# Kernel optimization log

Measured on AMD Instinct MI355X. Metric: run time of the kernel, lower is better.

The kernel has to match this reference:

```python
import jax, jax.numpy as jnp
import numpy as np

EPS = 1e-5

def _bn(x, g, b):
    # training-mode BatchNorm1d: batch statistics (biased variance), eps=1e-5
    mean = jnp.mean(x, axis=0)
    var = jnp.mean(jnp.square(x - mean), axis=0)
    return (x - mean) * jax.lax.rsqrt(var + EPS) * g + b

def setup_inputs() -> dict:
    key = jax.random.key(0)
    ks = jax.random.split(key, 16)
    n_nodes, n_edges, d_h, d_e = 50000, 800000, 128, 64
    in_feats, h1, h2, out_feats = 2 * d_h + d_e, 256, 128, 1
    def lin(k, fi, fo):
        bound = 1.0 / np.sqrt(fi)
        kw, kb = jax.random.split(k)
        W = jax.random.uniform(kw, (fo, fi), jnp.float32, -bound, bound)
        b = jax.random.uniform(kb, (fo,), jnp.float32, -bound, bound)
        return W, b
    W1, b1 = lin(ks[0], in_feats, h1)
    W2, b2 = lin(ks[1], h1, h2)
    W3, b3 = lin(ks[2], h2, out_feats)
    return {
        "h": jax.random.normal(ks[3], (n_nodes, d_h), jnp.float32),
        "e": jax.random.normal(ks[4], (n_edges, d_e), jnp.float32),
        "src": jax.random.randint(ks[5], (n_edges,), 0, n_nodes, jnp.int32),
        "dst": jax.random.randint(ks[6], (n_edges,), 0, n_nodes, jnp.int32),
        "bn0_g": jnp.ones((in_feats,), jnp.float32), "bn0_b": jnp.zeros((in_feats,), jnp.float32),
        "W1": W1, "b1": b1,
        "bn1_g": jnp.ones((h1,), jnp.float32), "bn1_b": jnp.zeros((h1,), jnp.float32),
        "W2": W2, "b2": b2,
        "bn2_g": jnp.ones((h2,), jnp.float32), "bn2_b": jnp.zeros((h2,), jnp.float32),
        "W3": W3, "b3": b3,
    }

def reference(h, e, src, dst, bn0_g, bn0_b, W1, b1, bn1_g, bn1_b, W2, b2, bn2_g, bn2_b, W3, b3):
    # edge gather + concat: [n_edges, 2*d_h + d_e]
    x = jnp.concatenate([h[src], h[dst], e], axis=1)
    x = _bn(x, bn0_g, bn0_b)
    x = jnp.maximum(x @ W1.T + b1, 0.0)  # Linear + ReLU (dropout = identity, deterministic)
    x = _bn(x, bn1_g, bn1_b)
    x = jnp.maximum(x @ W2.T + b2, 0.0)
    x = _bn(x, bn2_g, bn2_b)
    return x @ W3.T + b3
```

## Files before the change

### kernel.cpp

```cpp
#include <hip/hip_runtime.h>


#define N_EDGES 800000
#define N_NODES 50000

typedef __attribute__((ext_vector_type(8))) short bf8_t;
typedef __attribute__((ext_vector_type(4))) float f4_t;
typedef __attribute__((ext_vector_type(2))) unsigned int u2_t;
typedef __attribute__((ext_vector_type(4))) unsigned int u4_t;

__device__ __forceinline__ unsigned short f2bf(float f) {
    unsigned int u = __builtin_bit_cast(unsigned int, f);
    u += 0x7FFFu + ((u >> 16) & 1u);
    return (unsigned short)(u >> 16);
}
__device__ __forceinline__ float bf2f(unsigned short s) {
    unsigned int u = ((unsigned int)s) << 16;
    return __builtin_bit_cast(float, u);
}
__device__ __forceinline__ bf8_t cvt8(f4_t x, f4_t y) {
    bf8_t r;
    r[0] = (short)f2bf(x[0]); r[1] = (short)f2bf(x[1]);
    r[2] = (short)f2bf(x[2]); r[3] = (short)f2bf(x[3]);
    r[4] = (short)f2bf(y[0]); r[5] = (short)f2bf(y[1]);
    r[6] = (short)f2bf(y[2]); r[7] = (short)f2bf(y[3]);
    return r;
}

__global__ __launch_bounds__(256) void k_hist(const int* __restrict__ src, const int* __restrict__ dst,
                                              int* __restrict__ cs, int* __restrict__ cd) {
    int i = blockIdx.x * 256 + threadIdx.x;
    if (i < N_EDGES) {
        atomicAdd(&cs[src[i]], 1);
        atomicAdd(&cd[dst[i]], 1);
    }
}

__global__ __launch_bounds__(256) void k_ecvt(const float* __restrict__ e,
        unsigned short* __restrict__ ebf, float* __restrict__ sum, float* __restrict__ sq) {
    const int tid = threadIdx.x;
    const int lane = tid & 63;
    const int cg = tid & 7, rr = tid >> 3;
    f4_t sa = {0.f,0.f,0.f,0.f}, sb = sa, qa = sa, qb = sa;
    for (int r = blockIdx.x * 32 + rr; r < N_EDGES; r += gridDim.x * 32) {
        f4_t va = __builtin_nontemporal_load((const f4_t*)(e + (size_t)r * 64 + cg * 8));
        f4_t vb = __builtin_nontemporal_load((const f4_t*)(e + (size_t)r * 64 + cg * 8 + 4));
        sa += va; qa += va * va; sb += vb; qb += vb * vb;
        bf8_t o = cvt8(va, vb);
        __builtin_nontemporal_store(o,
            (bf8_t*)(ebf + (size_t)(r >> 4) * 1024 + (cg >> 2) * 512 + (((r & 15) << 2) + (cg & 3)) * 8));
    }
#pragma unroll
    for (int d = 8; d <= 32; d <<= 1) {
#pragma unroll
        for (int j = 0; j < 4; ++j) {
            sa[j] += __shfl_xor(sa[j], d); qa[j] += __shfl_xor(qa[j], d);
            sb[j] += __shfl_xor(sb[j], d); qb[j] += __shfl_xor(qb[j], d);
        }
    }
    __shared__ float red[128];
    if (tid < 128) red[tid] = 0.f;
    __syncthreads();
    if (lane < 8) {
#pragma unroll
        for (int j = 0; j < 4; ++j) {
            atomicAdd(&red[lane * 8 + j], sa[j]);
            atomicAdd(&red[lane * 8 + 4 + j], sb[j]);
            atomicAdd(&red[64 + lane * 8 + j], qa[j]);
            atomicAdd(&red[64 + lane * 8 + 4 + j], qb[j]);
        }
    }
    __syncthreads();
    if (tid < 64) atomicAdd(&sum[256 + tid], red[tid]);
    else if (tid < 128) atomicAdd(&sq[256 + tid - 64], red[tid]);
}

__global__ __launch_bounds__(256) void k_hstats(const float* __restrict__ h,
                                                const int* __restrict__ cs, const int* __restrict__ cd,
                                                float* __restrict__ sum, float* __restrict__ sq) {
    const int tid = threadIdx.x;
    const int c = tid & 127, g = tid >> 7;
    float ss = 0.f, qs = 0.f, sd = 0.f, qd = 0.f;
    for (int n = blockIdx.x * 2 + g; n < N_NODES; n += gridDim.x * 2) {
        float v = h[(size_t)n * 128 + c];
        float a = (float)cs[n], b = (float)cd[n];
        ss += a * v; qs += a * v * v;
        sd += b * v; qd += b * v * v;
    }
    __shared__ float red[256];
    red[tid] = ss; __syncthreads();
    if (tid < 128) atomicAdd(&sum[tid], red[tid] + red[tid + 128]);
    __syncthreads();
    red[tid] = qs; __syncthreads();
    if (tid < 128) atomicAdd(&sq[tid], red[tid] + red[tid + 128]);
    __syncthreads();
    red[tid] = sd; __syncthreads();
    if (tid < 128) atomicAdd(&sum[128 + tid], red[tid] + red[tid + 128]);
    __syncthreads();
    red[tid] = qd; __syncthreads();
    if (tid < 128) atomicAdd(&sq[128 + tid], red[tid] + red[tid + 128]);
}

__global__ __launch_bounds__(320) void k_fold0(const float* __restrict__ sum, const float* __restrict__ sq,
        const float* __restrict__ g0, const float* __restrict__ b0,
        float* __restrict__ scale0, float* __restrict__ shift0) {
    int j = threadIdx.x;
    if (j < 320) {
        const float invE = 1.f / (float)N_EDGES;
        float mu = sum[j] * invE;
        float var = sq[j] * invE - mu * mu;
        float sc = g0[j] * rsqrtf(var + 1e-5f);
        scale0[j] = sc;
        shift0[j] = b0[j] - mu * sc;
    }
}

__global__ __launch_bounds__(320) void k_foldW1(const float* __restrict__ W1, const float* __restrict__ b1,
        const float* __restrict__ scale0, const float* __restrict__ shift0,
        unsigned short* __restrict__ W1s, unsigned short* __restrict__ W1d,
        unsigned short* __restrict__ W1e, float* __restrict__ b1p) {
    __shared__ float sc[320], sh[320];
    const int tid = threadIdx.x;
    if (tid < 320) { sc[tid] = scale0[tid]; sh[tid] = shift0[tid]; }
    __syncthreads();
    if (tid < 256) {
        float acc = b1[tid];
        const float* wr = W1 + (size_t)tid * 320;
        for (int j = 0; j < 320; ++j) {
            float wv = wr[j];
            acc += wv * sh[j];
            unsigned short wb = f2bf(wv * sc[j]);
            if (j < 128) W1s[tid * 128 + j] = wb;
            else if (j < 256) W1d[tid * 128 + (j - 128)] = wb;
            else W1e[tid * 64 + (j - 256)] = wb;
        }
        b1p[tid] = acc;
    }
}

__global__ __launch_bounds__(256) void k_P(const float* __restrict__ h,
        const unsigned short* __restrict__ W1s, const unsigned short* __restrict__ W1d,
        unsigned short* __restrict__ Ps, unsigned short* __restrict__ Pd) {
    __shared__ unsigned short tile[16 * 264];
    const int tid = threadIdx.x;
    const int w = tid >> 6, lane = tid & 63, quad = lane >> 4, l15 = lane & 15;
    const unsigned short* W = blockIdx.y ? W1d : W1s;
    unsigned short* P = blockIdx.y ? Pd : Ps;
    const size_t base = (size_t)blockIdx.x * 256;
    bf8_t bfr[4][4];
#pragma unroll
    for (int j = 0; j < 4; ++j) {
        const unsigned short* wp = W + (size_t)((w * 4 + j) * 16 + l15) * 128 + quad * 8;
#pragma unroll
        for (int ks = 0; ks < 4; ++ks) bfr[j][ks] = *(const bf8_t*)(wp + ks * 32);
    }
    const int erow = tid >> 4, ex = tid & 15;
    for (int mc = 0; mc < 16; ++mc) {
        const size_t row0 = base + mc * 16;
        size_t ar = row0 + l15; if (ar >= N_NODES) ar = N_NODES - 1;
        const float* hp = h + ar * 128 + quad * 8;
        bf8_t af[4];
#pragma unroll
        for (int ks = 0; ks < 4; ++ks)
            af[ks] = cvt8(*(const f4_t*)(hp + ks * 32), *(const f4_t*)(hp + ks * 32 + 4));
#pragma unroll
        for (int j = 0; j < 4; ++j) {
            f4_t t = {0.f, 0.f, 0.f, 0.f};
#pragma unroll
            for (int ks = 0; ks < 4; ++ks)
                t = __builtin_amdgcn_mfma_f32_16x16x32_bf16(af[ks], bfr[j][ks], t, 0, 0, 0);
#pragma unroll
            for (int r = 0; r < 4; ++r)
                tile[(quad * 4 + r) * 264 + (w * 4 + j) * 16 + l15] = f2bf(t[r]);
        }
        __syncthreads();
        const size_t orow = row0 + erow;
        if (orow < N_NODES) {
            u4_t v0 = *(const u4_t*)(tile + erow * 264 + ex * 16);
            u4_t v1 = *(const u4_t*)(tile + erow * 264 + ex * 16 + 8);
            *(u4_t*)(P + orow * 256 + ex * 16) = v0;
            *(u4_t*)(P + orow * 256 + ex * 16 + 8) = v1;
        }
        __syncthreads();
    }
}

__global__ __launch_bounds__(256) void k_stats1(const unsigned short* __restrict__ ebf,
        const int* __restrict__ src, const int* __restrict__ dst,
        const unsigned short* __restrict__ Ps, const unsigned short* __restrict__ Pd,
        const unsigned short* __restrict__ W1e, const float* __restrict__ b1p,
        float* __restrict__ slots) {
    __shared__ int sIdx[256], dIdx[256];
    const int tid = threadIdx.x;
    const int w = tid >> 6, lane = tid & 63, quad = lane >> 4, l15 = lane & 15;
    const int perm = l15 * 4 + quad;
    const size_t base = (size_t)blockIdx.x * 256;
    const size_t blk16 = (size_t)blockIdx.x * 16;
    sIdx[tid] = src[base + tid];
    dIdx[tid] = dst[base + tid];
    bf8_t bfr[4][2];
    float bias4[4];
#pragma unroll
    for (int j = 0; j < 4; ++j) {
        const unsigned short* wp = W1e + (size_t)((w * 4 + j) * 16 + l15) * 64 + quad * 8;
        bfr[j][0] = *(const bf8_t*)(wp);
        bfr[j][1] = *(const bf8_t*)(wp + 32);
        bias4[j] = b1p[(w * 4 + j) * 16 + l15];
    }
    const int cb = w * 64 + l15;
    float s[4] = {0.f, 0.f, 0.f, 0.f}, q[4] = {0.f, 0.f, 0.f, 0.f};
    __syncthreads();
    bf8_t af0, af1;
    {
        const unsigned short* ap = ebf + blk16 * 1024 + perm * 8;
        af0 = __builtin_nontemporal_load((const bf8_t*)(ap));
        af1 = __builtin_nontemporal_load((const bf8_t*)(ap + 512));
    }
    for (int mc = 0; mc < 16; ++mc) {
        const int r0 = mc * 16 + quad * 4;
        const unsigned short* p0 = Ps + (size_t)sIdx[r0 + 0] * 256 + cb;
        const unsigned short* p1 = Ps + (size_t)sIdx[r0 + 1] * 256 + cb;
        const unsigned short* p2 = Ps + (size_t)sIdx[r0 + 2] * 256 + cb;
        const unsigned short* p3 = Ps + (size_t)sIdx[r0 + 3] * 256 + cb;
        const unsigned short* d0 = Pd + (size_t)dIdx[r0 + 0] * 256 + cb;
        const unsigned short* d1 = Pd + (size_t)dIdx[r0 + 1] * 256 + cb;
        const unsigned short* d2 = Pd + (size_t)dIdx[r0 + 2] * 256 + cb;
        const unsigned short* d3 = Pd + (size_t)dIdx[r0 + 3] * 256 + cb;
        unsigned short ps[4][4], pd[4][4];
#pragma unroll
        for (int j = 0; j < 4; ++j) {
            ps[0][j] = p0[j * 16]; ps[1][j] = p1[j * 16];
            ps[2][j] = p2[j * 16]; ps[3][j] = p3[j * 16];
            pd[0][j] = d0[j * 16]; pd[1][j] = d1[j * 16];
            pd[2][j] = d2[j * 16]; pd[3][j] = d3[j * 16];
        }
        f4_t acc[4];
#pragma unroll
        for (int j = 0; j < 4; ++j) {
            f4_t t = {bias4[j], bias4[j], bias4[j], bias4[j]};
            t = __builtin_amdgcn_mfma_f32_16x16x32_bf16(af0, bfr[j][0], t, 0, 0, 0);
            acc[j] = __builtin_amdgcn_mfma_f32_16x16x32_bf16(af1, bfr[j][1], t, 0, 0, 0);
        }
        if (mc < 15) {
            const unsigned short* ap = ebf + (blk16 + mc + 1) * 1024 + perm * 8;
            af0 = __builtin_nontemporal_load((const bf8_t*)(ap));
            af1 = __builtin_nontemporal_load((const bf8_t*)(ap + 512));
        }
#pragma unroll
        for (int j = 0; j < 4; ++j)
#pragma unroll
            for (int r = 0; r < 4; ++r) {
                float v = acc[j][r] + bf2f(ps[r][j]) + bf2f(pd[r][j]);
                v = fmaxf(v, 0.f);
                s[j] += v; q[j] += v * v;
            }
    }
#pragma unroll
    for (int j = 0; j < 4; ++j) {
        s[j] += __shfl_xor(s[j], 16); s[j] += __shfl_xor(s[j], 32);
        q[j] += __shfl_xor(q[j], 16); q[j] += __shfl_xor(q[j], 32);
    }
    if (lane < 16) {
        float* sl = slots + (size_t)(blockIdx.x & 63) * 512;
#pragma unroll
        for (int j = 0; j < 4; ++j) {
            atomicAdd(&sl[cb + j * 16], s[j]);
            atomicAdd(&sl[256 + cb + j * 16], q[j]);
        }
    }
}

__global__ __launch_bounds__(256) void k_fold1(const float* __restrict__ slots,
        const float* __restrict__ g1, const float* __restrict__ b1n,
        const float* __restrict__ W2, const float* __restrict__ b2,
        unsigned short* __restrict__ W2p, float* __restrict__ b2p) {
    __shared__ float sc[256], sh[256];
    const int tid = threadIdx.x;
    float S = 0.f, Q = 0.f;
    for (int s = 0; s < 64; ++s) { S += slots[s * 512 + tid]; Q += slots[s * 512 + 256 + tid]; }
    const float invE = 1.f / (float)N_EDGES;
    float mu = S * invE;
    float var = Q * invE - mu * mu;
    float scl = g1[tid] * rsqrtf(var + 1e-5f);
    sc[tid] = scl; sh[tid] = b1n[tid] - mu * scl;
    __syncthreads();
    if (tid < 128) {
        float acc = b2[tid];
        const float* wr = W2 + (size_t)tid * 256;
        for (int j = 0; j < 256; ++j) {
            float wv = wr[j];
            acc += wv * sh[j];
            W2p[tid * 256 + j] = f2bf(wv * sc[j]);
        }
        b2p[tid] = acc;
    }
}

__global__ __launch_bounds__(256) void k_L12(const unsigned short* __restrict__ ebf,
        const int* __restrict__ src, const int* __restrict__ dst,
        const unsigned short* __restrict__ Ps, const unsigned short* __restrict__ Pd,
        const unsigned short* __restrict__ W1e, const float* __restrict__ b1p,
        const unsigned short* __restrict__ W2p, const float* __restrict__ b2p,
        unsigned short* __restrict__ a2c, float* __restrict__ slots) {
    __shared__ __align__(16) float tile1[16 * 268];
    __shared__ unsigned short tile2[2][4096];
    __shared__ int sIdx[256], dIdx[256];
    const int tid = threadIdx.x;
    const int w = tid >> 6, lane = tid & 63, quad = lane >> 4, l15 = lane & 15;
    const int perm = l15 * 4 + quad;
    const size_t base = (size_t)blockIdx.x * 256;
    const size_t blk16 = (size_t)blockIdx.x * 16;
    sIdx[tid] = src[base + tid];
    dIdx[tid] = dst[base + tid];
    bf8_t bfr1[4][2];
    float bias4[4];
#pragma unroll
    for (int j = 0; j < 4; ++j) {
        const unsigned short* wp = W1e + (size_t)((w * 4 + j) * 16 + l15) * 64 + quad * 8;
        bfr1[j][0] = *(const bf8_t*)(wp);
        bfr1[j][1] = *(const bf8_t*)(wp + 32);
        bias4[j] = b1p[(w * 4 + j) * 16 + l15];
    }
    bf8_t bfr2[2][8];
    float bias2[2];
#pragma unroll
    for (int j = 0; j < 2; ++j) {
        const unsigned short* wp = W2p + (size_t)((w * 2 + j) * 16 + l15) * 256 + quad * 8;
#pragma unroll
        for (int ks = 0; ks < 8; ++ks) bfr2[j][ks] = *(const bf8_t*)(wp + ks * 32);
        bias2[j] = b2p[(w * 2 + j) * 16 + l15];
    }
    const int erow = tid >> 4, ex = tid & 15;
    float s0 = 0.f, q0 = 0.f, s1 = 0.f, q1 = 0.f;
    __syncthreads();
    bf8_t af0, af1;
    u4_t gs0, gs1, gd0, gd1;
    {
        const unsigned short* ap = ebf + blk16 * 1024 + perm * 8;
        af0 = __builtin_nontemporal_load((const bf8_t*)(ap));
        af1 = __builtin_nontemporal_load((const bf8_t*)(ap + 512));
        const size_t sr = (size_t)sIdx[erow] * 256, dr = (size_t)dIdx[erow] * 256;
        gs0 = *(const u4_t*)(Ps + sr + ex * 8);
        gs1 = *(const u4_t*)(Ps + sr + ex * 8 + 128);
        gd0 = *(const u4_t*)(Pd + dr + ex * 8);
        gd1 = *(const u4_t*)(Pd + dr + ex * 8 + 128);
    }
    for (int mc = 0; mc < 16; ++mc) {
        unsigned short* t2 = tile2[mc & 1];
#pragma unroll
        for (int j = 0; j < 4; ++j) {
            f4_t t = {bias4[j], bias4[j], bias4[j], bias4[j]};
            t = __builtin_amdgcn_mfma_f32_16x16x32_bf16(af0, bfr1[j][0], t, 0, 0, 0);
            t = __builtin_amdgcn_mfma_f32_16x16x32_bf16(af1, bfr1[j][1], t, 0, 0, 0);
#pragma unroll
            for (int r = 0; r < 4; ++r)
                tile1[(quad * 4 + r) * 268 + (w * 4 + j) * 16 + l15] = t[r];
        }
        if (mc < 15) {
            const unsigned short* ap = ebf + (blk16 + mc + 1) * 1024 + perm * 8;
            af0 = __builtin_nontemporal_load((const bf8_t*)(ap));
            af1 = __builtin_nontemporal_load((const bf8_t*)(ap + 512));
        }
        __syncthreads();
#pragma unroll
        for (int i = 0; i < 2; ++i) {
            const float* tp = tile1 + erow * 268 + ex * 8 + 128 * i;
            f4_t tv0 = *(const f4_t*)tp;
            f4_t tv1 = *(const f4_t*)(tp + 4);
            const unsigned short* su = (const unsigned short*)(i ? &gs1 : &gs0);
            const unsigned short* du = (const unsigned short*)(i ? &gd1 : &gd0);
            unsigned short ov[8];
#pragma unroll
            for (int j = 0; j < 4; ++j) {
                float v = tv0[j] + bf2f(su[j]) + bf2f(du[j]);
                ov[j] = f2bf(fmaxf(v, 0.f));
            }
#pragma unroll
            for (int j = 0; j < 4; ++j) {
                float v = tv1[j] + bf2f(su[4 + j]) + bf2f(du[4 + j]);
                ov[4 + j] = f2bf(fmaxf(v, 0.f));
            }
            *(u4_t*)(&t2[((ex >> 2) + 4 * i) * 512 + (erow * 4 + (ex & 3)) * 8]) = *(const u4_t*)ov;
        }
        if (mc < 15) {
            const size_t sr = (size_t)sIdx[(mc + 1) * 16 + erow] * 256;
            const size_t dr = (size_t)dIdx[(mc + 1) * 16 + erow] * 256;
            gs0 = *(const u4_t*)(Ps + sr + ex * 8);
            gs1 = *(const u4_t*)(Ps + sr + ex * 8 + 128);
            gd0 = *(const u4_t*)(Pd + dr + ex * 8);
            gd1 = *(const u4_t*)(Pd + dr + ex * 8 + 128);
        }
        __syncthreads();
        f4_t acc0 = {bias2[0], bias2[0], bias2[0], bias2[0]};
        f4_t acc1 = {bias2[1], bias2[1], bias2[1], bias2[1]};
#pragma unroll
        for (int ks = 0; ks < 8; ++ks) {
            bf8_t a = *(const bf8_t*)(&t2[ks * 512 + perm * 8]);
            acc0 = __builtin_amdgcn_mfma_f32_16x16x32_bf16(a, bfr2[0][ks], acc0, 0, 0, 0);
            acc1 = __builtin_amdgcn_mfma_f32_16x16x32_bf16(a, bfr2[1][ks], acc1, 0, 0, 0);
        }
        unsigned short* outp = a2c + (blk16 + mc) * 2048;
        unsigned short pv[4];
#pragma unroll
        for (int r = 0; r < 4; ++r) {
            float v = fmaxf(acc0[r], 0.f);
            pv[r] = f2bf(v); s0 += v; q0 += v * v;
        }
        __builtin_nontemporal_store(*(const u2_t*)pv,
            (u2_t*)(outp + (((w * 2) * 16 + l15) * 4 + quad) * 4));
#pragma unroll
        for (int r = 0; r < 4; ++r) {
            float v = fmaxf(acc1[r], 0.f);
            pv[r] = f2bf(v); s1 += v; q1 += v * v;
        }
        __builtin_nontemporal_store(*(const u2_t*)pv,
            (u2_t*)(outp + (((w * 2 + 1) * 16 + l15) * 4 + quad) * 4));
    }
    s0 += __shfl_xor(s0, 16); s0 += __shfl_xor(s0, 32);
    q0 += __shfl_xor(q0, 16); q0 += __shfl_xor(q0, 32);
    s1 += __shfl_xor(s1, 16); s1 += __shfl_xor(s1, 32);
    q1 += __shfl_xor(q1, 16); q1 += __shfl_xor(q1, 32);
    if (lane < 16) {
        float* sl = slots + (size_t)(blockIdx.x & 63) * 256;
        const int c0 = (w * 2) * 16 + l15;
        atomicAdd(&sl[c0], s0); atomicAdd(&sl[128 + c0], q0);
        atomicAdd(&sl[c0 + 16], s1); atomicAdd(&sl[128 + c0 + 16], q1);
    }
}

__global__ __launch_bounds__(128) void k_fold2(const float* __restrict__ slots,
        const float* __restrict__ g2, const float* __restrict__ b2n,
        const float* __restrict__ W3, const float* __restrict__ b3,
        float* __restrict__ w3p, float* __restrict__ b3p) {
    __shared__ float red[128];
    const int tid = threadIdx.x;
    float S = 0.f, Q = 0.f;
    for (int s = 0; s < 64; ++s) { S += slots[s * 256 + tid]; Q += slots[s * 256 + 128 + tid]; }
    const float invE = 1.f / (float)N_EDGES;
    float mu = S * invE;
    float var = Q * invE - mu * mu;
    float scl = g2[tid] * rsqrtf(var + 1e-5f);
    float shf = b2n[tid] - mu * scl;
    w3p[tid] = W3[tid] * scl;
    red[tid] = W3[tid] * shf;
    __syncthreads();
    for (int st = 64; st > 0; st >>= 1) {
        if (tid < st) red[tid] += red[tid + st];
        __syncthreads();
    }
    if (tid == 0) b3p[0] = b3[0] + red[0];
}

__global__ __launch_bounds__(256) void k_L3(const unsigned short* __restrict__ a2c,
        const float* __restrict__ w3p, const float* __restrict__ b3p, float* __restrict__ out) {
    __shared__ float wl[128];
    const int tid = threadIdx.x;
    if (tid < 128) wl[tid] = w3p[tid];
    __syncthreads();
    const int w = tid >> 6, lane = tid & 63, q = lane >> 4, c = lane & 15;
    const float bb = b3p[0];
#pragma unroll
    for (int i = 0; i < 4; ++i) {
        const size_t b = (size_t)blockIdx.x * 16 + w * 4 + i;
        const unsigned short* bp = a2c + b * 2048 + c * 16 + q * 4;
        float a0 = 0.f, a1r = 0.f, a2r = 0.f, a3r = 0.f;
#pragma unroll
        for (int jt = 0; jt < 8; ++jt) {
            u2_t v = __builtin_nontemporal_load((const u2_t*)(bp + jt * 256));
            const unsigned short* u = (const unsigned short*)&v;
            const float wv = wl[jt * 16 + c];
            a0 += bf2f(u[0]) * wv; a1r += bf2f(u[1]) * wv;
            a2r += bf2f(u[2]) * wv; a3r += bf2f(u[3]) * wv;
        }
#pragma unroll
        for (int d = 1; d <= 8; d <<= 1) {
            a0 += __shfl_xor(a0, d); a1r += __shfl_xor(a1r, d);
            a2r += __shfl_xor(a2r, d); a3r += __shfl_xor(a3r, d);
        }
        if (c == 0) {
            f4_t o = {a0 + bb, a1r + bb, a2r + bb, a3r + bb};
            *(f4_t*)(out + b * 16 + q * 4) = o;
        }
    }
}

extern "C" void kernel_launch(void* const* d_in, const int* in_sizes, int n_in,
                              void* d_out, int out_size, void* d_ws, size_t ws_size,
                              hipStream_t stream) {
    (void)in_sizes; (void)n_in; (void)out_size; (void)ws_size;
    const float* h   = (const float*)d_in[0];
    const float* e   = (const float*)d_in[1];
    const int*   src = (const int*)d_in[2];
    const int*   dst = (const int*)d_in[3];
    const float* bn0_g = (const float*)d_in[4];
    const float* bn0_b = (const float*)d_in[5];
    const float* W1 = (const float*)d_in[6];
    const float* b1 = (const float*)d_in[7];
    const float* bn1_g = (const float*)d_in[8];
    const float* bn1_b = (const float*)d_in[9];
    const float* W2 = (const float*)d_in[10];
    const float* b2 = (const float*)d_in[11];
    const float* bn2_g = (const float*)d_in[12];
    const float* bn2_b = (const float*)d_in[13];
    const float* W3 = (const float*)d_in[14];
    const float* b3 = (const float*)d_in[15];

    char* ws = (char*)d_ws;
    size_t off = 0;
    auto alloc = [&](size_t bytes) { char* p = ws + off; off += (bytes + 255) & ~(size_t)255; return p; };
    int*   cnt_s = (int*)alloc((size_t)N_NODES * 4);
    int*   cnt_d = (int*)alloc((size_t)N_NODES * 4);
    float* bn0_sum = (float*)alloc(320 * 4);
    float* bn0_sq  = (float*)alloc(320 * 4);
    float* bn1_slots = (float*)alloc(64 * 512 * 4);
    float* bn2_slots = (float*)alloc(64 * 256 * 4);
    const size_t zero_end = off;
    float* scale0 = (float*)alloc(320 * 4);
    float* shift0 = (float*)alloc(320 * 4);
    unsigned short* W1s = (unsigned short*)alloc(256 * 128 * 2);
    unsigned short* W1d = (unsigned short*)alloc(256 * 128 * 2);
    unsigned short* W1e = (unsigned short*)alloc(256 * 64 * 2);
    float* b1p = (float*)alloc(256 * 4);
    unsigned short* W2p = (unsigned short*)alloc(128 * 256 * 2);
    float* b2p = (float*)alloc(128 * 4);
    float* w3p = (float*)alloc(128 * 4);
    float* b3p = (float*)alloc(4);
    unsigned short* Ps = (unsigned short*)alloc((size_t)N_NODES * 256 * 2);
    unsigned short* Pd = (unsigned short*)alloc((size_t)N_NODES * 256 * 2);
    unsigned short* ebf = (unsigned short*)alloc((size_t)(N_EDGES / 16) * 2048);
    unsigned short* a2c = (unsigned short*)alloc((size_t)(N_EDGES / 16) * 4096);

    hipMemsetAsync(d_ws, 0, zero_end, stream);
    k_hist<<<(N_EDGES + 255) / 256, 256, 0, stream>>>(src, dst, cnt_s, cnt_d);
    k_ecvt<<<512, 256, 0, stream>>>(e, ebf, bn0_sum, bn0_sq);
    k_hstats<<<200, 256, 0, stream>>>(h, cnt_s, cnt_d, bn0_sum, bn0_sq);
    k_fold0<<<1, 320, 0, stream>>>(bn0_sum, bn0_sq, bn0_g, bn0_b, scale0, shift0);
    k_foldW1<<<1, 320, 0, stream>>>(W1, b1, scale0, shift0, W1s, W1d, W1e, b1p);
    k_P<<<dim3(196, 2), 256, 0, stream>>>(h, W1s, W1d, Ps, Pd);
    k_stats1<<<N_EDGES / 256, 256, 0, stream>>>(ebf, src, dst, Ps, Pd, W1e, b1p, bn1_slots);
    k_fold1<<<1, 256, 0, stream>>>(bn1_slots, bn1_g, bn1_b, W2, b2, W2p, b2p);
    k_L12<<<N_EDGES / 256, 256, 0, stream>>>(ebf, src, dst, Ps, Pd, W1e, b1p, W2p, b2p, a2c, bn2_slots);
    k_fold2<<<1, 128, 0, stream>>>(bn2_slots, bn2_g, bn2_b, W3, b3, w3p, b3p);
    k_L3<<<N_EDGES / 256, 256, 0, stream>>>(a2c, w3p, b3p, (float*)d_out);
}
```

Measured before the change: 1.161 ms.

## Coalesce node-projection gathers in stats1 via LDS-staged MFMA tile

Replaces the scattered 2-byte gathers of the per-node projections Ps/Pd with 16-byte vector loads per edge row, prefetched one chunk ahead. The MFMA outputs are staged through a double-buffered LDS tile so each thread's columns line up with its vectorized gather. The column statistics are then reduced across waves in LDS before one atomic per column. This adds a block barrier per chunk, about 34KB of LDS and more registers for 16 accumulators, which may lower occupancy.

```diff
diff --git a/kernel.cpp b/kernel.cpp
--- a/kernel.cpp
+++ b/kernel.cpp
@@ -190,6 +190,7 @@
         const unsigned short* __restrict__ Ps, const unsigned short* __restrict__ Pd,
         const unsigned short* __restrict__ W1e, const float* __restrict__ b1p,
         float* __restrict__ slots) {
+    __shared__ __align__(16) float tile1[2][16 * 268];
     __shared__ int sIdx[256], dIdx[256];
     const int tid = threadIdx.x;
     const int w = tid >> 6, lane = tid & 63, quad = lane >> 4, l15 = lane & 15;
@@ -198,75 +199,103 @@
     const size_t blk16 = (size_t)blockIdx.x * 16;
     sIdx[tid] = src[base + tid];
     dIdx[tid] = dst[base + tid];
-    bf8_t bfr[4][2];
+    bf8_t bfr1[4][2];
     float bias4[4];
 #pragma unroll
     for (int j = 0; j < 4; ++j) {
         const unsigned short* wp = W1e + (size_t)((w * 4 + j) * 16 + l15) * 64 + quad * 8;
-        bfr[j][0] = *(const bf8_t*)(wp);
-        bfr[j][1] = *(const bf8_t*)(wp + 32);
+        bfr1[j][0] = *(const bf8_t*)(wp);
+        bfr1[j][1] = *(const bf8_t*)(wp + 32);
         bias4[j] = b1p[(w * 4 + j) * 16 + l15];
     }
-    const int cb = w * 64 + l15;
-    float s[4] = {0.f, 0.f, 0.f, 0.f}, q[4] = {0.f, 0.f, 0.f, 0.f};
+    const int erow = tid >> 4, ex = tid & 15;
+    float s[16], q[16];
+#pragma unroll
+    for (int j = 0; j < 16; ++j) { s[j] = 0.f; q[j] = 0.f; }
     __syncthreads();
     bf8_t af0, af1;
+    u4_t gs0, gs1, gd0, gd1;
     {
         const unsigned short* ap = ebf + blk16 * 1024 + perm * 8;
         af0 = __builtin_nontemporal_load((const bf8_t*)(ap));
         af1 = __builtin_nontemporal_load((const bf8_t*)(ap + 512));
+        const size_t sr = (size_t)sIdx[erow] * 256, dr = (size_t)dIdx[erow] * 256;
+        gs0 = *(const u4_t*)(Ps + sr + ex * 8);
+        gs1 = *(const u4_t*)(Ps + sr + ex * 8 + 128);
+        gd0 = *(const u4_t*)(Pd + dr + ex * 8);
+        gd1 = *(const u4_t*)(Pd + dr + ex * 8 + 128);
     }
     for (int mc = 0; mc < 16; ++mc) {
-        const int r0 = mc * 16 + quad * 4;
-        const unsigned short* p0 = Ps + (size_t)sIdx[r0 + 0] * 256 + cb;
-        const unsigned short* p1 = Ps + (size_t)sIdx[r0 + 1] * 256 + cb;
-        const unsigned short* p2 = Ps + (size_t)sIdx[r0 + 2] * 256 + cb;
-        const unsigned short* p3 = Ps + (size_t)sIdx[r0 + 3] * 256 + cb;
-        const unsigned short* d0 = Pd + (size_t)dIdx[r0 + 0] * 256 + cb;
-        const unsigned short* d1 = Pd + (size_t)dIdx[r0 + 1] * 256 + cb;
-        const unsigned short* d2 = Pd + (size_t)dIdx[r0 + 2] * 256 + cb;
-        const unsigned short* d3 = Pd + (size_t)dIdx[r0 + 3] * 256 + cb;
-        unsigned short ps[4][4], pd[4][4];
-#pragma unroll
-        for (int j = 0; j < 4; ++j) {
-            ps[0][j] = p0[j * 16]; ps[1][j] = p1[j * 16];
-            ps[2][j] = p2[j * 16]; ps[3][j] = p3[j * 16];
-            pd[0][j] = d0[j * 16]; pd[1][j] = d1[j * 16];
-            pd[2][j] = d2[j * 16]; pd[3][j] = d3[j * 16];
-        }
-        f4_t acc[4];
+        float* t1 = tile1[mc & 1];
 #pragma unroll
         for (int j = 0; j < 4; ++j) {
             f4_t t = {bias4[j], bias4[j], bias4[j], bias4[j]};
-            t = __builtin_amdgcn_mfma_f32_16x16x32_bf16(af0, bfr[j][0], t, 0, 0, 0);
-            acc[j] = __builtin_amdgcn_mfma_f32_16x16x32_bf16(af1, bfr[j][1], t, 0, 0, 0);
+            t = __builtin_amdgcn_mfma_f32_16x16x32_bf16(af0, bfr1[j][0], t, 0, 0, 0);
+            t = __builtin_amdgcn_mfma_f32_16x16x32_bf16(af1, bfr1[j][1], t, 0, 0, 0);
+#pragma unroll
+            for (int r = 0; r < 4; ++r)
+                t1[(quad * 4 + r) * 268 + (w * 4 + j) * 16 + l15] = t[r];
         }
         if (mc < 15) {
             const unsigned short* ap = ebf + (blk16 + mc + 1) * 1024 + perm * 8;
             af0 = __builtin_nontemporal_load((const bf8_t*)(ap));
             af1 = __builtin_nontemporal_load((const bf8_t*)(ap + 512));
         }
-#pragma unroll
-        for (int j = 0; j < 4; ++j)
-#pragma unroll
-            for (int r = 0; r < 4; ++r) {
-                float v = acc[j][r] + bf2f(ps[r][j]) + bf2f(pd[r][j]);
-                v = fmaxf(v, 0.f);
-                s[j] += v; q[j] += v * v;
+        __syncthreads();
+#pragma unroll
+        for (int i = 0; i < 2; ++i) {
+            const float* tp = t1 + erow * 268 + ex * 8 + 128 * i;
+            f4_t tv0 = *(const f4_t*)tp;
+            f4_t tv1 = *(const f4_t*)(tp + 4);
+            const unsigned short* su = (const unsigned short*)(i ? &gs1 : &gs0);
+            const unsigned short* du = (const unsigned short*)(i ? &gd1 : &gd0);
+#pragma unroll
+            for (int j = 0; j < 4; ++j) {
+                float v = fmaxf(tv0[j] + bf2f(su[j]) + bf2f(du[j]), 0.f);
+                s[i * 8 + j] += v; q[i * 8 + j] += v * v;
             }
-    }
-#pragma unroll
-    for (int j = 0; j < 4; ++j) {
+#pragma unroll
+            for (int j = 0; j < 4; ++j) {
+                float v = fmaxf(tv1[j] + bf2f(su[4 + j]) + bf2f(du[4 + j]), 0.f);
+                s[i * 8 + 4 + j] += v; q[i * 8 + 4 + j] += v * v;
+            }
+        }
+        if (mc < 15) {
+            const size_t sr = (size_t)sIdx[(mc + 1) * 16 + erow] * 256;
+            const size_t dr = (size_t)dIdx[(mc + 1) * 16 + erow] * 256;
+            gs0 = *(const u4_t*)(Ps + sr + ex * 8);
+            gs1 = *(const u4_t*)(Ps + sr + ex * 8 + 128);
+            gd0 = *(const u4_t*)(Pd + dr + ex * 8);
+            gd1 = *(const u4_t*)(Pd + dr + ex * 8 + 128);
+        }
+    }
+#pragma unroll
+    for (int j = 0; j < 16; ++j) {
         s[j] += __shfl_xor(s[j], 16); s[j] += __shfl_xor(s[j], 32);
         q[j] += __shfl_xor(q[j], 16); q[j] += __shfl_xor(q[j], 32);
     }
+    float* scratch = &tile1[0][0];
     if (lane < 16) {
+#pragma unroll
+        for (int j = 0; j < 16; ++j) {
+            scratch[(w * 16 + l15) * 16 + j] = s[j];
+            scratch[1024 + (w * 16 + l15) * 16 + j] = q[j];
+        }
+    }
+    __syncthreads();
+    {
+        const int c = tid;
+        const int idx = (c & 7) + (c >> 7) * 8;
+        const int exx = (c >> 3) & 15;
+        float S = 0.f, Q = 0.f;
+#pragma unroll
+        for (int ww = 0; ww < 4; ++ww) {
+            S += scratch[(ww * 16 + exx) * 16 + idx];
+            Q += scratch[1024 + (ww * 16 + exx) * 16 + idx];
+        }
         float* sl = slots + (size_t)(blockIdx.x & 63) * 512;
-#pragma unroll
-        for (int j = 0; j < 4; ++j) {
-            atomicAdd(&sl[cb + j * 16], s[j]);
-            atomicAdd(&sl[256 + cb + j * 16], q[j]);
-        }
+        atomicAdd(&sl[c], S);
+        atomicAdd(&sl[256 + c], Q);
     }
 }
 
```

Measured after the change: 1.022 ms. 12.0% less time.
